# Performance work log

Measured on AMD Instinct MI355X. Metric: run time of the kernel, lower is better.

Reference implementation:

```python
import jax, jax.numpy as jnp
import numpy as np


def setup_inputs() -> dict:
    key = jax.random.key(0)
    k1, k2, k3, k4 = jax.random.split(key, 4)
    B, T, C, H = 16, 2048, 1024, 128
    x = jax.random.normal(k1, (B, T, C), dtype=jnp.float32)
    # bias-free Dense kernels (stored as [in, out] like keras)
    s = 1.0 / np.sqrt(C)
    Wk = jax.random.normal(k2, (C, H), dtype=jnp.float32) * s
    Wq = jax.random.normal(k3, (C, H), dtype=jnp.float32) * s
    Wv = jax.random.normal(k4, (C, H), dtype=jnp.float32) * s
    return {"x": x, "Wk": Wk, "Wq": Wq, "Wv": Wv}


def reference(x, Wk, Wq, Wv):
    # single-head causal self-attention (dropout inactive at inference)
    B, T, C = x.shape
    H = Wk.shape[-1]
    k = jnp.einsum('btc,ch->bth', x, Wk)   # [B,T,H]
    q = jnp.einsum('btc,ch->bth', x, Wq)
    v = jnp.einsum('btc,ch->bth', x, Wv)
    scale = 1.0 / jnp.sqrt(jnp.float32(H))
    wei = jnp.einsum('bqh,bkh->bqk', q, k) * scale          # [B,T,T]
    causal = jnp.tril(jnp.ones((T, T), dtype=bool))
    wei = jnp.where(causal, wei, -jnp.inf)
    wei = jax.nn.softmax(wei, axis=-1)
    out = jnp.einsum('bqk,bkh->bqh', wei, v)                # [B,T,H]
    return out
```

## Files before the change

### kernel.cpp

```cpp
#include <hip/hip_runtime.h>
#include <hip/hip_bf16.h>

typedef __bf16 bf16x8_t __attribute__((ext_vector_type(8)));
typedef __bf16 bf16x4_t __attribute__((ext_vector_type(4)));
typedef float  f32x4_t  __attribute__((ext_vector_type(4)));

#define MFMA_16x16x32_BF16(A, B, C) __builtin_amdgcn_mfma_f32_16x16x32_bf16((A), (B), (C), 0, 0, 0)

static constexpr int B_ = 16;
static constexpr int T_ = 2048;
static constexpr int C_ = 1024;
static constexpr int H_ = 128;
static constexpr long M_ = (long)B_ * T_;

__device__ __forceinline__ void gload_lds16(const void* g, void* l)
{
    __builtin_amdgcn_global_load_lds(
        (const __attribute__((address_space(1))) void*)g,
        (__attribute__((address_space(3))) void*)l, 16, 0, 0);
}

__global__ __launch_bounds__(128) void wt_kernel(
    const float* __restrict__ Wq, const float* __restrict__ Wk,
    const float* __restrict__ Wv, __bf16* __restrict__ WT)
{
    const int z = blockIdx.y;
    const float* __restrict__ W = (z == 0) ? Wq : (z == 1) ? Wk : Wv;
    const int h  = threadIdx.x;
    const int c0 = blockIdx.x * 8;
    bf16x8_t v;
    #pragma unroll
    for (int j = 0; j < 8; ++j)
        v[j] = (__bf16)W[(c0 + j) * H_ + h];
    *(bf16x8_t*)&WT[((long)z * H_ + h) * C_ + c0] = v;
}

__global__ __launch_bounds__(512, 4) void proj_kernel(
    const float*  __restrict__ x,
    const __bf16* __restrict__ WT,
    __bf16* __restrict__ qo,
    __bf16* __restrict__ ko,
    __bf16* __restrict__ vo)
{
    __shared__ __bf16 XS[2][64 * 32];
    __shared__ __bf16 WS[2][384 * 32];

    const int tid  = threadIdx.x;
    const int w    = tid >> 6;
    const int lane = tid & 63;
    const int m16  = lane & 15;
    const int quad = lane >> 4;
    const int koff = quad * 8;
    const int mt   = w >> 1;
    const int nh   = w & 1;

    const long r0 = (long)blockIdx.x * 64;

    const int xrow = tid >> 3, xc = tid & 7;
    const int wrow = lane >> 2, wcol = lane & 3;

    f32x4_t acc[12];
    #pragma unroll
    for (int j = 0; j < 12; ++j) acc[j] = f32x4_t{0, 0, 0, 0};

    {
        f32x4_t xv = *(const f32x4_t*)&x[(r0 + xrow) * C_ + xc * 4];
        #pragma unroll
        for (int ch = 0; ch < 3; ++ch) {
            const int rowb = w * 48 + ch * 16;
            gload_lds16(&WT[(long)(rowb + wrow) * C_ + wcol * 8],
                        &WS[0][rowb * 32]);
        }
        bf16x4_t xb;
        #pragma unroll
        for (int j = 0; j < 4; ++j) xb[j] = (__bf16)xv[j];
        *(bf16x4_t*)&XS[0][xrow * 32 + xc * 4] = xb;
    }
    __syncthreads();

    for (int t = 0; t < 32; ++t) {
        const int cur = t & 1, nxt = cur ^ 1;
        const int k0n = (t + 1) * 32;

        f32x4_t xv;
        if (t < 31) {
            xv = *(const f32x4_t*)&x[(r0 + xrow) * C_ + k0n + xc * 4];
            #pragma unroll
            for (int ch = 0; ch < 3; ++ch) {
                const int rowb = w * 48 + ch * 16;
                gload_lds16(&WT[(long)(rowb + wrow) * C_ + k0n + wcol * 8],
                            &WS[nxt][rowb * 32]);
            }
        }

        bf16x8_t a = *(const bf16x8_t*)&XS[cur][(mt * 16 + m16) * 32 + koff];
        #pragma unroll
        for (int j = 0; j < 12; ++j) {
            bf16x8_t bfr =
                *(const bf16x8_t*)&WS[cur][((nh * 12 + j) * 16 + m16) * 32 + koff];
            acc[j] = MFMA_16x16x32_BF16(a, bfr, acc[j]);
        }

        if (t < 31) {
            bf16x4_t xb;
            #pragma unroll
            for (int j = 0; j < 4; ++j) xb[j] = (__bf16)xv[j];
            *(bf16x4_t*)&XS[nxt][xrow * 32 + xc * 4] = xb;
        }
        __syncthreads();
    }

    const long rbase = r0 + mt * 16 + quad * 4;
    #pragma unroll
    for (int j = 0; j < 12; ++j) {
        const int ntg = nh * 12 + j;
        const int z = ntg >> 3;
        const int h = (ntg & 7) * 16 + m16;
        if (z < 2) {
            __bf16* __restrict__ o = z ? ko : qo;
            #pragma unroll
            for (int r = 0; r < 4; ++r)
                o[(rbase + r) * H_ + h] = (__bf16)acc[j][r];
        } else {
            long bb = rbase >> 11, tt = rbase & 2047;
            bf16x4_t pk;
            #pragma unroll
            for (int r = 0; r < 4; ++r) pk[r] = (__bf16)acc[j][r];
            *(bf16x4_t*)&vo[bb * (H_ * (long)T_) + h * (long)T_ + tt] = pk;
        }
    }
}

__global__ __launch_bounds__(256) void attn_kernel(
    const __bf16* __restrict__ q,
    const __bf16* __restrict__ k,
    const __bf16* __restrict__ vT,
    float* __restrict__ out)
{
    __shared__ __bf16 KS[64 * 136];
    __shared__ __bf16 VS[128 * 72];
    __shared__ __bf16 PS[4][16 * 72];

    const int L   = blockIdx.x;
    const int b   = L & 15;
    const int Lh  = L >> 4;
    const int qb  = (Lh < 16) ? (31 - Lh) : (Lh - 16);

    const int tid  = threadIdx.x;
    const int w    = tid >> 6;
    const int lane = tid & 63;
    const int m16  = lane & 15;
    const int quad = lane >> 4;
    const int koff = quad * 8;

    const __bf16* __restrict__ qp = q  + (long)b * T_ * H_;
    const __bf16* __restrict__ kp = k  + (long)b * T_ * H_;
    const __bf16* __restrict__ vp = vT + (long)b * H_ * T_;

    const int q0w = qb * 64 + w * 16;
    const int qg  = q0w + m16;

    bf16x8_t qfr[4];
    #pragma unroll
    for (int s = 0; s < 4; ++s)
        qfr[s] = *(const bf16x8_t*)&qp[(q0w + m16) * H_ + s * 32 + koff];

    f32x4_t acc[8];
    #pragma unroll
    for (int i = 0; i < 8; ++i) acc[i] = f32x4_t{0, 0, 0, 0};
    float mrun = -1e30f, lrun = 0.f;

    __bf16* Pb = &PS[w][0];
    const float SC = 0.08838834764831845f;
    const int kend = qb * 64 + 64;

    const int krow = tid >> 4, kc16 = tid & 15;
    const int vrow = tid >> 3, vc8  = tid & 7;

    for (int tk0 = 0; tk0 < kend; tk0 += 64) {
        __syncthreads();
        #pragma unroll
        for (int ch = 0; ch < 4; ++ch) {
            int r = krow + ch * 16;
            *(bf16x8_t*)&KS[r * 136 + kc16 * 8] =
                *(const bf16x8_t*)&kp[(tk0 + r) * H_ + kc16 * 8];
        }
        #pragma unroll
        for (int ch = 0; ch < 4; ++ch) {
            int hh = vrow + ch * 32;
            *(bf16x8_t*)&VS[hh * 72 + vc8 * 8] =
                *(const bf16x8_t*)&vp[hh * (long)T_ + tk0 + vc8 * 8];
        }
        __syncthreads();

        f32x4_t st[4];
        #pragma unroll
        for (int kt = 0; kt < 4; ++kt) {
            f32x4_t s = f32x4_t{0, 0, 0, 0};
            #pragma unroll
            for (int sI = 0; sI < 4; ++sI) {
                bf16x8_t kf = *(const bf16x8_t*)&KS[(kt * 16 + m16) * 136 + sI * 32 + koff];
                s = MFMA_16x16x32_BF16(kf, qfr[sI], s);
            }
            st[kt] = s;
        }

        float vv[4][4];
        if (tk0 + 63 <= q0w) {
            #pragma unroll
            for (int kt = 0; kt < 4; ++kt)
                #pragma unroll
                for (int r = 0; r < 4; ++r)
                    vv[kt][r] = st[kt][r] * SC;
        } else {
            #pragma unroll
            for (int kt = 0; kt < 4; ++kt)
                #pragma unroll
                for (int r = 0; r < 4; ++r) {
                    int kg = tk0 + kt * 16 + quad * 4 + r;
                    vv[kt][r] = (kg <= qg) ? st[kt][r] * SC : -1e30f;
                }
        }

        float mloc = -1e30f;
        #pragma unroll
        for (int kt = 0; kt < 4; ++kt)
            #pragma unroll
            for (int r = 0; r < 4; ++r)
                mloc = fmaxf(mloc, vv[kt][r]);
        mloc = fmaxf(mloc, __shfl_xor(mloc, 16, 64));
        mloc = fmaxf(mloc, __shfl_xor(mloc, 32, 64));

        float mnew = fmaxf(mrun, mloc);
        float al   = __expf(mrun - mnew);
        float psum = 0.f;
        #pragma unroll
        for (int kt = 0; kt < 4; ++kt) {
            bf16x4_t pk;
            #pragma unroll
            for (int r = 0; r < 4; ++r) {
                float p = __expf(vv[kt][r] - mnew);
                psum += p;
                pk[r] = (__bf16)p;
            }
            *(bf16x4_t*)&Pb[m16 * 72 + kt * 16 + quad * 4] = pk;
        }
        psum += __shfl_xor(psum, 16, 64);
        psum += __shfl_xor(psum, 32, 64);
        mrun = mnew;
        lrun = lrun * al + psum;

        #pragma unroll
        for (int i = 0; i < 8; ++i)
            #pragma unroll
            for (int r = 0; r < 4; ++r)
                acc[i][r] *= al;

        #pragma unroll
        for (int half = 0; half < 2; ++half) {
            bf16x8_t pa = *(const bf16x8_t*)&Pb[m16 * 72 + half * 32 + koff];
            #pragma unroll
            for (int i = 0; i < 8; ++i) {
                bf16x8_t vf = *(const bf16x8_t*)&VS[(i * 16 + m16) * 72 + half * 32 + koff];
                acc[i] = MFMA_16x16x32_BF16(vf, pa, acc[i]);
            }
        }
    }

    float* __restrict__ ob = out + (long)b * T_ * H_;
    const float inv = 1.f / lrun;
    #pragma unroll
    for (int i = 0; i < 8; ++i) {
        f32x4_t o;
        #pragma unroll
        for (int r = 0; r < 4; ++r) o[r] = acc[i][r] * inv;
        *(f32x4_t*)&ob[(q0w + m16) * H_ + i * 16 + quad * 4] = o;
    }
}

extern "C" void kernel_launch(void* const* d_in, const int* in_sizes, int n_in,
                              void* d_out, int out_size, void* d_ws, size_t ws_size,
                              hipStream_t stream)
{
    const float* x  = (const float*)d_in[0];
    const float* Wk = (const float*)d_in[1];
    const float* Wq = (const float*)d_in[2];
    const float* Wv = (const float*)d_in[3];

    __bf16* qws = (__bf16*)d_ws;
    __bf16* kws = qws + M_ * H_;
    __bf16* vws = kws + M_ * H_;
    __bf16* WT  = vws + (long)B_ * H_ * T_;
    float*  out = (float*)d_out;

    wt_kernel  <<<dim3(C_ / 8, 3), 128, 0, stream>>>(Wq, Wk, Wv, WT);
    proj_kernel<<<dim3((int)(M_ / 64)), 512, 0, stream>>>(x, WT, qws, kws, vws);
    attn_kernel<<<dim3(512), 256, 0, stream>>>(qws, kws, vws, out);
}
```

Before: 291.9 us.

## Load x directly to LDS as fp32 with swizzle and 2x6 warp tiling

The projection kernel now loads x with async global-to-LDS copies in fp32 instead of through registers, and converts to bf16 when fragments are read from LDS. It adds XOR swizzles on the x and W tiles to avoid LDS bank conflicts, and remaps waves so each computes 2 row tiles by 6 column tiles, reusing each B fragment across two MFMAs. Explicit vmcnt waits and raw barriers replace __syncthreads so prefetches overlap compute. The fp32 x tile doubles its LDS footprint, and the conversion now runs in the inner loop for every wave.

```diff
diff --git a/kernel.cpp b/kernel.cpp
--- a/kernel.cpp
+++ b/kernel.cpp
@@ -42,8 +42,124 @@
     __bf16* __restrict__ ko,
     __bf16* __restrict__ vo)
 {
-    __shared__ __bf16 XS[2][64 * 32];
+    __shared__ float  XS[2][64 * 32];
     __shared__ __bf16 WS[2][384 * 32];
+
+    const int tid  = threadIdx.x;
+    const int w    = tid >> 6;
+    const int lane = tid & 63;
+    const int m16  = lane & 15;
+    const int quad = lane >> 4;
+    const int mt2  = w >> 2;
+    const int nq   = w & 3;
+
+    const long r0 = (long)blockIdx.x * 64;
+
+    const int xrow = tid >> 3;
+    const int xcol = ((tid & 7) ^ (xrow & 7)) << 2;
+    const int wrr  = lane >> 2;
+    const int wqc  = ((lane & 3) ^ ((lane >> 3) & 3)) << 3;
+
+    f32x4_t acc[2][6];
+    #pragma unroll
+    for (int hh = 0; hh < 2; ++hh)
+        #pragma unroll
+        for (int j = 0; j < 6; ++j) acc[hh][j] = f32x4_t{0, 0, 0, 0};
+
+    gload_lds16(&x[(r0 + xrow) * C_ + xcol], &XS[0][w * 8 * 32]);
+    #pragma unroll
+    for (int ch = 0; ch < 3; ++ch) {
+        const int rowb = w * 48 + ch * 16;
+        gload_lds16(&WT[(long)(rowb + wrr) * C_ + wqc], &WS[0][rowb * 32]);
+    }
+
+    for (int t = 0; t < 32; ++t) {
+        const int cur = t & 1, nxt = cur ^ 1;
+        const int k0n = (t + 1) * 32;
+
+        if (t < 31) {
+            gload_lds16(&x[(r0 + xrow) * C_ + k0n + xcol], &XS[nxt][w * 8 * 32]);
+            #pragma unroll
+            for (int ch = 0; ch < 3; ++ch) {
+                const int rowb = w * 48 + ch * 16;
+                gload_lds16(&WT[(long)(rowb + wrr) * C_ + k0n + wqc],
+                            &WS[nxt][rowb * 32]);
+            }
+            __builtin_amdgcn_sched_barrier(0);
+            asm volatile("s_waitcnt vmcnt(4)" ::: "memory");
+        } else {
+            __builtin_amdgcn_sched_barrier(0);
+            asm volatile("s_waitcnt vmcnt(0)" ::: "memory");
+        }
+        __builtin_amdgcn_s_barrier();
+        __builtin_amdgcn_sched_barrier(0);
+
+        bf16x8_t a[2];
+        #pragma unroll
+        for (int hh = 0; hh < 2; ++hh) {
+            const int row = mt2 * 32 + hh * 16 + m16;
+            const int sw  = m16 & 7;
+            f32x4_t lo = *(const f32x4_t*)&XS[cur][row * 32 + (((quad * 2 + 0) ^ sw) << 2)];
+            f32x4_t hi = *(const f32x4_t*)&XS[cur][row * 32 + (((quad * 2 + 1) ^ sw) << 2)];
+            #pragma unroll
+            for (int jj = 0; jj < 4; ++jj) {
+                a[hh][jj]     = (__bf16)lo[jj];
+                a[hh][4 + jj] = (__bf16)hi[jj];
+            }
+        }
+        const int qsw = (quad ^ ((m16 >> 1) & 3)) << 3;
+        #pragma unroll
+        for (int j = 0; j < 6; ++j) {
+            const int row = (nq * 6 + j) * 16 + m16;
+            bf16x8_t b = *(const bf16x8_t*)&WS[cur][row * 32 + qsw];
+            acc[0][j] = MFMA_16x16x32_BF16(a[0], b, acc[0][j]);
+            acc[1][j] = MFMA_16x16x32_BF16(a[1], b, acc[1][j]);
+        }
+
+        __builtin_amdgcn_sched_barrier(0);
+        asm volatile("s_waitcnt lgkmcnt(0)" ::: "memory");
+        __builtin_amdgcn_s_barrier();
+        __builtin_amdgcn_sched_barrier(0);
+    }
+
+    #pragma unroll
+    for (int hh = 0; hh < 2; ++hh) {
+        const long rbase = r0 + mt2 * 32 + hh * 16 + quad * 4;
+        #pragma unroll
+        for (int j = 0; j < 6; ++j) {
+            const int nt = nq * 6 + j;
+            const int z  = nt >> 3;
+            const int h  = (nt & 7) * 16 + m16;
+            if (z < 2) {
+                __bf16* __restrict__ o = z ? ko : qo;
+                #pragma unroll
+                for (int r = 0; r < 4; ++r)
+                    o[(rbase + r) * H_ + h] = (__bf16)acc[hh][j][r];
+            } else {
+                long bb = rbase >> 11, tt = rbase & 2047;
+                bf16x4_t pk;
+                #pragma unroll
+                for (int r = 0; r < 4; ++r) pk[r] = (__bf16)acc[hh][j][r];
+                *(bf16x4_t*)&vo[bb * (H_ * (long)T_) + h * (long)T_ + tt] = pk;
+            }
+        }
+    }
+}
+
+__global__ __launch_bounds__(256) void attn_kernel(
+    const __bf16* __restrict__ q,
+    const __bf16* __restrict__ k,
+    const __bf16* __restrict__ vT,
+    float* __restrict__ out)
+{
+    __shared__ __bf16 KS[64 * 136];
+    __shared__ __bf16 VS[128 * 72];
+    __shared__ __bf16 PS[4][16 * 72];
+
+    const int L   = blockIdx.x;
+    const int b   = L & 15;
+    const int Lh  = L >> 4;
+    const int qb  = (Lh < 16) ? (31 - Lh) : (Lh - 16);
 
     const int tid  = threadIdx.x;
     const int w    = tid >> 6;
@@ -51,107 +167,6 @@
     const int m16  = lane & 15;
     const int quad = lane >> 4;
     const int koff = quad * 8;
-    const int mt   = w >> 1;
-    const int nh   = w & 1;
-
-    const long r0 = (long)blockIdx.x * 64;
-
-    const int xrow = tid >> 3, xc = tid & 7;
-    const int wrow = lane >> 2, wcol = lane & 3;
-
-    f32x4_t acc[12];
-    #pragma unroll
-    for (int j = 0; j < 12; ++j) acc[j] = f32x4_t{0, 0, 0, 0};
-
-    {
-        f32x4_t xv = *(const f32x4_t*)&x[(r0 + xrow) * C_ + xc * 4];
-        #pragma unroll
-        for (int ch = 0; ch < 3; ++ch) {
-            const int rowb = w * 48 + ch * 16;
-            gload_lds16(&WT[(long)(rowb + wrow) * C_ + wcol * 8],
-                        &WS[0][rowb * 32]);
-        }
-        bf16x4_t xb;
-        #pragma unroll
-        for (int j = 0; j < 4; ++j) xb[j] = (__bf16)xv[j];
-        *(bf16x4_t*)&XS[0][xrow * 32 + xc * 4] = xb;
-    }
-    __syncthreads();
-
-    for (int t = 0; t < 32; ++t) {
-        const int cur = t & 1, nxt = cur ^ 1;
-        const int k0n = (t + 1) * 32;
-
-        f32x4_t xv;
-        if (t < 31) {
-            xv = *(const f32x4_t*)&x[(r0 + xrow) * C_ + k0n + xc * 4];
-            #pragma unroll
-            for (int ch = 0; ch < 3; ++ch) {
-                const int rowb = w * 48 + ch * 16;
-                gload_lds16(&WT[(long)(rowb + wrow) * C_ + k0n + wcol * 8],
-                            &WS[nxt][rowb * 32]);
-            }
-        }
-
-        bf16x8_t a = *(const bf16x8_t*)&XS[cur][(mt * 16 + m16) * 32 + koff];
-        #pragma unroll
-        for (int j = 0; j < 12; ++j) {
-            bf16x8_t bfr =
-                *(const bf16x8_t*)&WS[cur][((nh * 12 + j) * 16 + m16) * 32 + koff];
-            acc[j] = MFMA_16x16x32_BF16(a, bfr, acc[j]);
-        }
-
-        if (t < 31) {
-            bf16x4_t xb;
-            #pragma unroll
-            for (int j = 0; j < 4; ++j) xb[j] = (__bf16)xv[j];
-            *(bf16x4_t*)&XS[nxt][xrow * 32 + xc * 4] = xb;
-        }
-        __syncthreads();
-    }
-
-    const long rbase = r0 + mt * 16 + quad * 4;
-    #pragma unroll
-    for (int j = 0; j < 12; ++j) {
-        const int ntg = nh * 12 + j;
-        const int z = ntg >> 3;
-        const int h = (ntg & 7) * 16 + m16;
-        if (z < 2) {
-            __bf16* __restrict__ o = z ? ko : qo;
-            #pragma unroll
-            for (int r = 0; r < 4; ++r)
-                o[(rbase + r) * H_ + h] = (__bf16)acc[j][r];
-        } else {
-            long bb = rbase >> 11, tt = rbase & 2047;
-            bf16x4_t pk;
-            #pragma unroll
-            for (int r = 0; r < 4; ++r) pk[r] = (__bf16)acc[j][r];
-            *(bf16x4_t*)&vo[bb * (H_ * (long)T_) + h * (long)T_ + tt] = pk;
-        }
-    }
-}
-
-__global__ __launch_bounds__(256) void attn_kernel(
-    const __bf16* __restrict__ q,
-    const __bf16* __restrict__ k,
-    const __bf16* __restrict__ vT,
-    float* __restrict__ out)
-{
-    __shared__ __bf16 KS[64 * 136];
-    __shared__ __bf16 VS[128 * 72];
-    __shared__ __bf16 PS[4][16 * 72];
-
-    const int L   = blockIdx.x;
-    const int b   = L & 15;
-    const int Lh  = L >> 4;
-    const int qb  = (Lh < 16) ? (31 - Lh) : (Lh - 16);
-
-    const int tid  = threadIdx.x;
-    const int w    = tid >> 6;
-    const int lane = tid & 63;
-    const int m16  = lane & 15;
-    const int quad = lane >> 4;
-    const int koff = quad * 8;
 
     const __bf16* __restrict__ qp = q  + (long)b * T_ * H_;
     const __bf16* __restrict__ kp = k  + (long)b * T_ * H_;
```

Result: no change. 290.6 us (-0.4%).
